# Kernel tuning notes

Hardware: AMD Instinct MI355X
Metric: run time of the kernel (lower is better)

Reference implementation:

```python
import jax, jax.numpy as jnp
import numpy as np

# ---- Pin(3,0,1)-equivariant linear basis (gatr-style): 9 maps of shape (16,16).
# Blade order: [1, e0,e1,e2,e3, e01,e02,e03,e12,e13,e23, e012,e013,e023,e123, e0123]
# 5 grade projections + 4 left-multiplication-by-e0 maps (unit coefficients).
def _build_basis():
    grades = [[0], [1, 2, 3, 4], [5, 6, 7, 8, 9, 10], [11, 12, 13, 14], [15]]
    maps = []
    for g in grades:
        m = np.zeros((16, 16), np.float32)
        m[g, g] = 1.0
        maps.append(m)
    e0_pairs = [[(1, 0)], [(5, 2), (6, 3), (7, 4)], [(11, 8), (12, 9), (13, 10)], [(15, 14)]]
    for pairs in e0_pairs:
        m = np.zeros((16, 16), np.float32)
        for dst, src in pairs:
            m[dst, src] = 1.0
        maps.append(m)
    return jnp.asarray(np.stack(maps))  # (9, 16, 16): basis[y, x_out, a_in]

BASIS = _build_basis()
NUM_HEADS, HID_MV, HID_S = 8, 8, 32

def equi_linear(mv, s, w_mv, w_s2mv, w_mv2s, w_s2s, b_s):
    # mv: (..., N, Cin, 16); s: (..., N, Sin)
    out_mv = jnp.einsum('yxa,oiy,...ia->...ox', BASIS, w_mv, mv)
    out_mv = out_mv.at[..., 0].add(jnp.einsum('...i,oi->...o', s, w_s2mv))
    out_s = (jnp.einsum('...i,oi->...o', mv[..., 0], w_mv2s)
             + jnp.einsum('...i,oi->...o', s, w_s2s) + b_s)
    return out_mv, out_s

def split_heads_mv(x):  # (..., N, hid*H, 16) -> (..., H, N, hid, 16)
    x = x.reshape(*x.shape[:-2], HID_MV, NUM_HEADS, 16)
    return jnp.moveaxis(x, -2, -4)

def split_heads_s(x):  # (..., N, hid*H) -> (..., H, N, hid)
    x = x.reshape(*x.shape[:-1], HID_S, NUM_HEADS)
    return jnp.moveaxis(x, -1, -3)

def split_kv_mv(x):  # (..., N, 2*hid*H, 16) -> (2, ..., H, N, hid, 16)
    x = x.reshape(*x.shape[:-2], 2, HID_MV, NUM_HEADS, 16)
    x = jnp.moveaxis(x, -4, 0)
    return jnp.moveaxis(x, -2, -4)

def split_kv_s(x):  # (..., N, 2*hid*H) -> (2, ..., H, N, hid)
    x = x.reshape(*x.shape[:-1], 2, HID_S, NUM_HEADS)
    x = jnp.moveaxis(x, -3, 0)
    return jnp.moveaxis(x, -1, -3)

def setup_inputs() -> dict:
    key = jax.random.key(0)
    ks = jax.random.split(key, 14)
    B, N, C_MV, C_S = 2, 4096, 32, 128
    sc = 0.05
    return {
        'inputs': jax.random.normal(ks[0], (B, N, C_MV, 16), jnp.float32),
        'scalars': jax.random.normal(ks[1], (B, N, C_S), jnp.float32),
        'q_w_mv': jax.random.normal(ks[2], (HID_MV * NUM_HEADS, C_MV, 9)) * sc,
        'q_w_s2mv': jax.random.normal(ks[3], (HID_MV * NUM_HEADS, C_S)) * sc,
        'q_w_mv2s': jax.random.normal(ks[4], (HID_S * NUM_HEADS, C_MV)) * sc,
        'q_w_s2s': jax.random.normal(ks[5], (HID_S * NUM_HEADS, C_S)) * sc,
        'q_b_s': jnp.zeros((HID_S * NUM_HEADS,), jnp.float32),
        'kv_w_mv': jax.random.normal(ks[6], (2 * HID_MV * NUM_HEADS, C_MV, 9)) * sc,
        'kv_w_s2mv': jax.random.normal(ks[7], (2 * HID_MV * NUM_HEADS, C_S)) * sc,
        'kv_w_mv2s': jax.random.normal(ks[8], (2 * HID_S * NUM_HEADS, C_MV)) * sc,
        'kv_w_s2s': jax.random.normal(ks[9], (2 * HID_S * NUM_HEADS, C_S)) * sc,
        'kv_b_s': jnp.zeros((2 * HID_S * NUM_HEADS,), jnp.float32),
        'q_idx': jax.random.randint(ks[10], (N,), 0, N),
        'kv_idx': jax.random.randint(ks[11], (N,), 0, N),
    }

def reference(inputs, scalars, q_w_mv, q_w_s2mv, q_w_mv2s, q_w_s2s, q_b_s,
              kv_w_mv, kv_w_s2mv, kv_w_mv2s, kv_w_s2s, kv_b_s, q_idx, kv_idx):
    # to_queries / to_keys = item-axis gathers (cross-attention selection)
    q_in = jnp.take(inputs, q_idx, axis=-3)
    q_sc = jnp.take(scalars, q_idx, axis=-2)
    q_mv, q_s = equi_linear(q_in, q_sc, q_w_mv, q_w_s2mv, q_w_mv2s, q_w_s2s, q_b_s)
    q_mv = split_heads_mv(q_mv)
    q_s = split_heads_s(q_s)

    kv_mv, kv_s = equi_linear(inputs, scalars, kv_w_mv, kv_w_s2mv, kv_w_mv2s, kv_w_s2s, kv_b_s)
    k_mv, v_mv = split_kv_mv(jnp.take(kv_mv, kv_idx, axis=-3))
    v_mv_queries = split_kv_mv(jnp.take(kv_mv, q_idx, axis=-3))[1]
    k_s, v_s = split_kv_s(jnp.take(kv_s, kv_idx, axis=-2))
    v_s_queries = split_kv_s(jnp.take(kv_s, q_idx, axis=-2))[1]
    return (q_mv, k_mv, v_mv, v_mv_queries, q_s, k_s, v_s, v_s_queries)
```

## Files before the change

kernel.cpp:

```cpp
#include <hip/hip_runtime.h>
#include <hip/hip_bf16.h>
#include <stdint.h>

typedef short bf16x8 __attribute__((ext_vector_type(8)));
typedef short bf16x2 __attribute__((ext_vector_type(2)));
typedef float f32x4 __attribute__((ext_vector_type(4)));

#define NN 4096

static __device__ __forceinline__ short f2b(float f) {
    union { float f; uint32_t u; } a; a.f = f;
    uint32_t r = a.u + 0x7FFFu + ((a.u >> 16) & 1u);
    return (short)(r >> 16);
}

#define OFF_QMV   0UL
#define OFF_KMV   8388608UL
#define OFF_VMV   16777216UL
#define OFF_VMVQ  25165824UL
#define OFF_QS    33554432UL
#define OFF_KS    35651584UL
#define OFF_VS    37748736UL
#define OFF_VSQ   39845888UL

#define WS_BMV_END   73728
#define WS_SW_BASE   106496
#define WS_PACK_END  270336

static __device__ __forceinline__ int mv_chan(int ct, int l) {
    return (ct >> 2) * 64 + (l & 7) * 8 + (ct & 3) * 2 + ((l >> 3) & 1);
}

static __device__ __forceinline__ int s_chan(int ct, int lr) {
    int hid = (ct & 3) + 4 * (lr >> 3) + 8 * (ct >> 2);
    return (lr & 7) + 8 * hid;
}

__global__ __launch_bounds__(256) void prep_pack(
    const float* __restrict__ qwmv,   const float* __restrict__ qws2mv,
    const float* __restrict__ qwmv2s, const float* __restrict__ qws2s,
    const float* __restrict__ kvwmv,  const float* __restrict__ kvws2mv,
    const float* __restrict__ kvwmv2s,const float* __restrict__ kvws2s,
    short* __restrict__ ws)
{
    const int id = blockIdx.x * 256 + threadIdx.x;
    if (id >= WS_PACK_END) return;
    float v;
    if (id < WS_BMV_END) {
        int rem = id; int task = rem / 36864; rem -= task * 36864;
        int y = rem / 4096; rem -= y * 4096;
        int ct = rem >> 9; int l = (rem >> 3) & 63; int e = rem & 7;
        int o = mv_chan(ct, l);
        int i = (l >> 4) * 8 + e;
        const float* w = (task == 0 || o >= 64) ? kvwmv : qwmv;
        v = w[(o * 32 + i) * 9 + y];
    } else if (id < WS_SW_BASE) {
        int rem = id - WS_BMV_END; int task = rem / 16384; rem -= task * 16384;
        int kk = rem / 4096; rem -= kk * 4096;
        int ct = rem >> 9; int l = (rem >> 3) & 63; int e = rem & 7;
        int o = mv_chan(ct, l);
        int k = kk * 32 + (l >> 4) * 8 + e;
        const float* w = (task == 0 || o >= 64) ? kvws2mv : qws2mv;
        v = w[o * 128 + k];
    } else {
        int rem = id - WS_SW_BASE; int task = rem / 81920; rem -= task * 81920;
        int ct = rem / 2560; rem -= ct * 2560;
        int lr = rem / 160;  int k = rem - lr * 160;
        int o = s_chan(ct, lr);
        if (k < 32) {
            const float* w = (task == 0 || o >= 256) ? kvwmv2s : qwmv2s;
            v = w[o * 32 + k];
        } else {
            const float* w = (task == 0 || o >= 256) ? kvws2s : qws2s;
            v = w[o * 128 + (k - 32)];
        }
    }
    ws[id] = f2b(v);
}

__global__ __launch_bounds__(256) void fused_all(
    const float* __restrict__ inputs, const float* __restrict__ scalars,
    const float* __restrict__ q_b_s,  const float* __restrict__ kv_b_s,
    const int* __restrict__ q_idx,    const int* __restrict__ kv_idx,
    const short* __restrict__ ws,     float* __restrict__ out)
{
    const int GR[16]   = {0,1,1,1,1,2,2,2,2,2,2,3,3,3,3,4};
    const int SRC[16]  = {-1,0,-1,-1,-1,2,3,4,-1,-1,-1,8,9,10,-1,14};
    const int EMAP[16] = {0,5,0,0,0,6,6,6,0,0,0,7,7,7,0,8};

    __shared__ __align__(16) char SMEM[65536];
    short* XA = (short*)SMEM;
    short* XS = XA + 16 * 520;

    const int tid  = threadIdx.x;
    const int bid  = blockIdx.x;
    const int tile = bid & 255;
    const int b    = (bid >> 8) & 1;
    const int task = bid >> 9;
    const int n0   = tile * 16;
    const int* ridx = task ? q_idx : kv_idx;

    {
        const int r = tid >> 4, c = tid & 15;
        const int m = ridx[n0 + r];
        const float* arow = inputs + (size_t)(b * NN + m) * 512;
        short t2[2][16];
        #pragma unroll
        for (int ii = 0; ii < 2; ++ii)
            #pragma unroll
            for (int q = 0; q < 4; ++q) {
                const float4 v = *(const float4*)(arow + (2 * c + ii) * 16 + q * 4);
                t2[ii][q * 4 + 0] = f2b(v.x); t2[ii][q * 4 + 1] = f2b(v.y);
                t2[ii][q * 4 + 2] = f2b(v.z); t2[ii][q * 4 + 3] = f2b(v.w);
            }
        #pragma unroll
        for (int x = 0; x < 16; ++x) {
            bf16x2 pr = {t2[0][x], t2[1][x]};
            *(bf16x2*)(XA + r * 520 + x * 32 + 2 * c) = pr;
        }
        const float* srow = scalars + (size_t)(b * NN + m) * 128 + c * 8;
        const float4 s0 = *(const float4*)(srow);
        const float4 s1 = *(const float4*)(srow + 4);
        bf16x8 sv = {f2b(s0.x), f2b(s0.y), f2b(s0.z), f2b(s0.w),
                     f2b(s1.x), f2b(s1.y), f2b(s1.z), f2b(s1.w)};
        *(bf16x8*)(XS + r * 136 + c * 8) = sv;
    }
    __syncthreads();

    const int w  = tid >> 6;
    const int l  = tid & 63;
    const int lr = l & 15;
    const int lg = l >> 4;

    bf16x8 Ax[16];
    #pragma unroll
    for (int x = 0; x < 16; ++x)
        Ax[x] = *(const bf16x8*)(XA + lr * 520 + x * 32 + lg * 8);
    bf16x8 Sx[4];
    #pragma unroll
    for (int kk = 0; kk < 4; ++kk)
        Sx[kk] = *(const bf16x8*)(XS + lr * 136 + kk * 32 + lg * 8);
    __syncthreads();

    float* OUTw = (float*)SMEM + w * 4096;

    #pragma unroll
    for (int cc = 0; cc < 2; ++cc) {
        const int ct = 2 * w + cc;
        bf16x8 Bg[9];
        #pragma unroll
        for (int y = 0; y < 9; ++y)
            Bg[y] = *(const bf16x8*)(ws + ((((size_t)task * 9 + y) * 8 + ct) * 64 + l) * 8);

        #pragma unroll
        for (int xc = 0; xc < 4; ++xc) {
            f32x4 acc[4];
            #pragma unroll
            for (int q = 0; q < 4; ++q) {
                const int x = xc * 4 + q;
                f32x4 a0 = {0.f, 0.f, 0.f, 0.f};
                a0 = __builtin_amdgcn_mfma_f32_16x16x32_bf16(Ax[x], Bg[GR[x]], a0, 0, 0, 0);
                if (SRC[x] >= 0)
                    a0 = __builtin_amdgcn_mfma_f32_16x16x32_bf16(Ax[SRC[x]], Bg[EMAP[x]], a0, 0, 0, 0);
                if (x == 0) {
                    #pragma unroll
                    for (int kk = 0; kk < 4; ++kk) {
                        bf16x8 bs2 = *(const bf16x8*)(ws + WS_BMV_END +
                                       ((((size_t)task * 4 + kk) * 8 + ct) * 64 + l) * 8);
                        a0 = __builtin_amdgcn_mfma_f32_16x16x32_bf16(Sx[kk], bs2, a0, 0, 0, 0);
                    }
                }
                acc[q] = a0;
            }
            #pragma unroll
            for (int j = 0; j < 4; ++j) {
                const int roww = (lr >> 3) * 16 + lg * 4 + j;
                const int cqw  = ((lr & 7) * 4 + xc) ^ ((roww >> 2) & 7);
                *(f32x4*)(OUTw + roww * 128 + cqw * 4) =
                    (f32x4){acc[0][j], acc[1][j], acc[2][j], acc[3][j]};
            }
        }

        const int region = ct >> 2;
        const size_t obase = task ? (region ? OFF_VMVQ : OFF_QMV)
                                  : (region ? OFF_VMV  : OFF_KMV);
        #pragma unroll
        for (int t = 0; t < 16; ++t) {
            const int row  = 2 * t + (l >> 5);
            const int h2   = row >> 4, nl = row & 15;
            const int head = (ct & 3) * 2 + h2;
            const int cq   = (l & 31) ^ ((row >> 2) & 7);
            f32x4 v = *(const f32x4*)(OUTw + row * 128 + cq * 4);
            __builtin_nontemporal_store(v,
                (f32x4*)(out + obase + (((size_t)(b * 8 + head)) * NN + n0 + nl) * 128
                         + (l & 31) * 4));
        }
    }

    __syncthreads();
    float* OUTS = (float*)SMEM;

    #pragma unroll
    for (int q8 = 0; q8 < 2; ++q8) {
        const int hidbase = 16 * w + 8 * q8 + 4 * (lr >> 3);
        const int head    = lr & 7;
        const int hq      = hidbase >> 2;
        const int region  = w >> 1;
        f32x4 acc4[4];
        #pragma unroll
        for (int jj = 0; jj < 4; ++jj) {
            const int ct = w * 8 + q8 * 4 + jj;
            const short* bp = ws + WS_SW_BASE +
                              (((size_t)task * 32 + ct) * 16 + lr) * 160 + lg * 8;
            f32x4 acc = {0.f, 0.f, 0.f, 0.f};
            acc = __builtin_amdgcn_mfma_f32_16x16x32_bf16(Ax[0], *(const bf16x8*)bp, acc, 0, 0, 0);
            #pragma unroll
            for (int c = 0; c < 4; ++c)
                acc = __builtin_amdgcn_mfma_f32_16x16x32_bf16(
                          Sx[c], *(const bf16x8*)(bp + 32 + c * 32), acc, 0, 0, 0);
            acc4[jj] = acc;
        }
        float bs[4];
        #pragma unroll
        for (int jj = 0; jj < 4; ++jj) {
            const int o = head + 8 * (hidbase + jj);
            bs[jj] = (task == 0) ? kv_b_s[o] : ((o < 256) ? q_b_s[o] : kv_b_s[o]);
        }
        const int c = (hq & 7) ^ head;
        #pragma unroll
        for (int j = 0; j < 4; ++j) {
            const int R = region * 128 + head * 16 + lg * 4 + j;
            *(f32x4*)(OUTS + R * 32 + c * 4) =
                (f32x4){acc4[0][j] + bs[0], acc4[1][j] + bs[1],
                        acc4[2][j] + bs[2], acc4[3][j] + bs[3]};
        }
    }
    __syncthreads();

    {
        const int region = w >> 1;
        const size_t obase = task ? (region ? OFF_VSQ : OFF_QS)
                                  : (region ? OFF_VS  : OFF_KS);
        #pragma unroll
        for (int k = 0; k < 8; ++k) {
            const int head = (w & 1) * 4 + (k & 3);
            const int nl   = (k >> 2) * 8 + (l >> 3);
            const int q    = l & 7;
            f32x4 v = *(const f32x4*)(OUTS + ((region * 128 + head * 16 + nl)) * 32
                                      + ((q ^ head) & 7) * 4);
            __builtin_nontemporal_store(v,
                (f32x4*)(out + obase + (((size_t)(b * 8 + head)) * NN + n0 + nl) * 32
                         + q * 4));
        }
    }
}

extern "C" void kernel_launch(void* const* d_in, const int* in_sizes, int n_in,
                              void* d_out, int out_size, void* d_ws, size_t ws_size,
                              hipStream_t stream) {
    const float* inputs  = (const float*)d_in[0];
    const float* scalars = (const float*)d_in[1];
    const float* qwmv    = (const float*)d_in[2];
    const float* qws2mv  = (const float*)d_in[3];
    const float* qwmv2s  = (const float*)d_in[4];
    const float* qws2s   = (const float*)d_in[5];
    const float* qbs     = (const float*)d_in[6];
    const float* kvwmv   = (const float*)d_in[7];
    const float* kvws2mv = (const float*)d_in[8];
    const float* kvwmv2s = (const float*)d_in[9];
    const float* kvws2s  = (const float*)d_in[10];
    const float* kvbs    = (const float*)d_in[11];
    const int*   qidx    = (const int*)d_in[12];
    const int*   kvidx   = (const int*)d_in[13];
    short* ws   = (short*)d_ws;
    float* outp = (float*)d_out;

    prep_pack<<<(WS_PACK_END + 255) / 256, 256, 0, stream>>>(
        qwmv, qws2mv, qwmv2s, qws2s, kvwmv, kvws2mv, kvwmv2s, kvws2s, ws);

    fused_all<<<1024, 256, 0, stream>>>(
        inputs, scalars, qbs, kvbs, qidx, kvidx, ws, outp);
}
```

Before: 49.54 us.

## Halve block to two waves with per-wave private LDS and fewer barriers

The fused kernel now runs 128 threads (2 waves) per block instead of 256, and each wave handles twice as many channel tiles. Shared memory drops to 32 KB, which can allow more resident blocks per CU. Because each wave now owns its own LDS staging region for output and scalar results, two block-wide barriers are removed. The trade-off is less parallelism per tile and more serial MFMA and store work per wave, with possible register pressure from the larger unrolled loops.

```diff
diff --git a/kernel.cpp b/kernel.cpp
--- a/kernel.cpp
+++ b/kernel.cpp
@@ -3,7 +3,7 @@
 #include <stdint.h>
 
 typedef short bf16x8 __attribute__((ext_vector_type(8)));
-typedef short bf16x2 __attribute__((ext_vector_type(2)));
+typedef short bf16x4 __attribute__((ext_vector_type(4)));
 typedef float f32x4 __attribute__((ext_vector_type(4)));
 
 #define NN 4096
@@ -78,7 +78,7 @@
     ws[id] = f2b(v);
 }
 
-__global__ __launch_bounds__(256) void fused_all(
+__global__ __launch_bounds__(128) void fused_all(
     const float* __restrict__ inputs, const float* __restrict__ scalars,
     const float* __restrict__ q_b_s,  const float* __restrict__ kv_b_s,
     const int* __restrict__ q_idx,    const int* __restrict__ kv_idx,
@@ -88,7 +88,7 @@
     const int SRC[16]  = {-1,0,-1,-1,-1,2,3,4,-1,-1,-1,8,9,10,-1,14};
     const int EMAP[16] = {0,5,0,0,0,6,6,6,0,0,0,7,7,7,0,8};
 
-    __shared__ __align__(16) char SMEM[65536];
+    __shared__ __align__(16) char SMEM[32768];
     short* XA = (short*)SMEM;
     short* XS = XA + 16 * 520;
 
@@ -101,29 +101,32 @@
     const int* ridx = task ? q_idx : kv_idx;
 
     {
-        const int r = tid >> 4, c = tid & 15;
+        const int r = tid >> 3, c = tid & 7;
         const int m = ridx[n0 + r];
         const float* arow = inputs + (size_t)(b * NN + m) * 512;
-        short t2[2][16];
-        #pragma unroll
-        for (int ii = 0; ii < 2; ++ii)
+        short t4[4][16];
+        #pragma unroll
+        for (int ii = 0; ii < 4; ++ii)
             #pragma unroll
             for (int q = 0; q < 4; ++q) {
-                const float4 v = *(const float4*)(arow + (2 * c + ii) * 16 + q * 4);
-                t2[ii][q * 4 + 0] = f2b(v.x); t2[ii][q * 4 + 1] = f2b(v.y);
-                t2[ii][q * 4 + 2] = f2b(v.z); t2[ii][q * 4 + 3] = f2b(v.w);
+                const float4 v = *(const float4*)(arow + (4 * c + ii) * 16 + q * 4);
+                t4[ii][q * 4 + 0] = f2b(v.x); t4[ii][q * 4 + 1] = f2b(v.y);
+                t4[ii][q * 4 + 2] = f2b(v.z); t4[ii][q * 4 + 3] = f2b(v.w);
             }
         #pragma unroll
         for (int x = 0; x < 16; ++x) {
-            bf16x2 pr = {t2[0][x], t2[1][x]};
-            *(bf16x2*)(XA + r * 520 + x * 32 + 2 * c) = pr;
-        }
-        const float* srow = scalars + (size_t)(b * NN + m) * 128 + c * 8;
-        const float4 s0 = *(const float4*)(srow);
-        const float4 s1 = *(const float4*)(srow + 4);
-        bf16x8 sv = {f2b(s0.x), f2b(s0.y), f2b(s0.z), f2b(s0.w),
-                     f2b(s1.x), f2b(s1.y), f2b(s1.z), f2b(s1.w)};
-        *(bf16x8*)(XS + r * 136 + c * 8) = sv;
+            bf16x4 pr = {t4[0][x], t4[1][x], t4[2][x], t4[3][x]};
+            *(bf16x4*)(XA + r * 520 + x * 32 + 4 * c) = pr;
+        }
+        const float* srow = scalars + (size_t)(b * NN + m) * 128 + c * 16;
+        #pragma unroll
+        for (int h = 0; h < 2; ++h) {
+            const float4 s0 = *(const float4*)(srow + h * 8);
+            const float4 s1 = *(const float4*)(srow + h * 8 + 4);
+            bf16x8 sv = {f2b(s0.x), f2b(s0.y), f2b(s0.z), f2b(s0.w),
+                         f2b(s1.x), f2b(s1.y), f2b(s1.z), f2b(s1.w)};
+            *(bf16x8*)(XS + r * 136 + c * 16 + h * 8) = sv;
+        }
     }
     __syncthreads();
 
@@ -145,8 +148,8 @@
     float* OUTw = (float*)SMEM + w * 4096;
 
     #pragma unroll
-    for (int cc = 0; cc < 2; ++cc) {
-        const int ct = 2 * w + cc;
+    for (int cc = 0; cc < 4; ++cc) {
+        const int ct = 4 * w + cc;
         bf16x8 Bg[9];
         #pragma unroll
         for (int y = 0; y < 9; ++y)
@@ -197,19 +200,17 @@
         }
     }
 
-    __syncthreads();
     float* OUTS = (float*)SMEM;
 
     #pragma unroll
-    for (int q8 = 0; q8 < 2; ++q8) {
-        const int hidbase = 16 * w + 8 * q8 + 4 * (lr >> 3);
+    for (int q8 = 0; q8 < 4; ++q8) {
+        const int hidbase = 32 * w + 8 * q8 + 4 * (lr >> 3);
         const int head    = lr & 7;
         const int hq      = hidbase >> 2;
-        const int region  = w >> 1;
         f32x4 acc4[4];
         #pragma unroll
         for (int jj = 0; jj < 4; ++jj) {
-            const int ct = w * 8 + q8 * 4 + jj;
+            const int ct = w * 16 + q8 * 4 + jj;
             const short* bp = ws + WS_SW_BASE +
                               (((size_t)task * 32 + ct) * 16 + lr) * 160 + lg * 8;
             f32x4 acc = {0.f, 0.f, 0.f, 0.f};
@@ -229,24 +230,22 @@
         const int c = (hq & 7) ^ head;
         #pragma unroll
         for (int j = 0; j < 4; ++j) {
-            const int R = region * 128 + head * 16 + lg * 4 + j;
+            const int R = w * 128 + head * 16 + lg * 4 + j;
             *(f32x4*)(OUTS + R * 32 + c * 4) =
                 (f32x4){acc4[0][j] + bs[0], acc4[1][j] + bs[1],
                         acc4[2][j] + bs[2], acc4[3][j] + bs[3]};
         }
     }
-    __syncthreads();
 
     {
-        const int region = w >> 1;
-        const size_t obase = task ? (region ? OFF_VSQ : OFF_QS)
-                                  : (region ? OFF_VS  : OFF_KS);
-        #pragma unroll
-        for (int k = 0; k < 8; ++k) {
-            const int head = (w & 1) * 4 + (k & 3);
-            const int nl   = (k >> 2) * 8 + (l >> 3);
+        const size_t obase = task ? (w ? OFF_VSQ : OFF_QS)
+                                  : (w ? OFF_VS  : OFF_KS);
+        #pragma unroll
+        for (int k = 0; k < 16; ++k) {
+            const int head = k & 7;
+            const int nl   = (k >> 3) * 8 + (l >> 3);
             const int q    = l & 7;
-            f32x4 v = *(const f32x4*)(OUTS + ((region * 128 + head * 16 + nl)) * 32
+            f32x4 v = *(const f32x4*)(OUTS + ((w * 128 + head * 16 + nl)) * 32
                                       + ((q ^ head) & 7) * 4);
             __builtin_nontemporal_store(v,
                 (f32x4*)(out + obase + (((size_t)(b * 8 + head)) * NN + n0 + nl) * 32
@@ -278,6 +277,6 @@
     prep_pack<<<(WS_PACK_END + 255) / 256, 256, 0, stream>>>(
         qwmv, qws2mv, qwmv2s, qws2s, kvwmv, kvws2mv, kvwmv2s, kvws2s, ws);
 
-    fused_all<<<1024, 256, 0, stream>>>(
+    fused_all<<<1024, 128, 0, stream>>>(
         inputs, scalars, qbs, kvbs, qidx, kvidx, ws, outp);
 }
```

Measured after the change: 46.51 us. -6.1%, faster.
